# Kernel optimization log

Measured on AMD Instinct MI355X. Metric: run time of the kernel, lower is better.

## Reference

```python
import jax, jax.numpy as jnp
import numpy as np

N_BATCH, N_SEQ, N_CHANNELS = 32, 4096, 128
N_EXPERTS, TOP_K = 64, 2
D_IN = 2 * N_SEQ  # linear input width


def setup_inputs() -> dict:
    key = jax.random.key(0)
    k_x, k_wm, k_bm, k_wn, k_bn = jax.random.split(key, 5)
    scale = 1.0 / np.sqrt(D_IN)  # torch nn.Linear default init range
    return {
        "x": jax.random.normal(k_x, (N_BATCH, N_SEQ, N_CHANNELS, 2), dtype=jnp.float32),
        "W_main": jax.random.uniform(k_wm, (N_EXPERTS, D_IN), jnp.float32, -scale, scale),
        "b_main": jax.random.uniform(k_bm, (N_EXPERTS,), jnp.float32, -scale, scale),
        "W_noise": jax.random.uniform(k_wn, (N_EXPERTS, D_IN), jnp.float32, -scale, scale),
        "b_noise": jax.random.uniform(k_bn, (N_EXPERTS,), jnp.float32, -scale, scale),
    }


def _keep_top_k(logits, k):
    # torch.kthvalue(x, n-k) = (n-k)-th smallest (1-based) = sorted[:, n-k-1]
    n = logits.shape[1]
    if n < k:
        return logits
    kth = jnp.sort(logits, axis=1)[:, n - k - 1:n - k]  # [rows, 1]
    return jnp.where(logits > kth, logits, -jnp.inf)


def reference(x, W_main, b_main, W_noise, b_noise):
    n_batch, n_seq, n_channels, _ = x.shape
    # swapaxes(1,2) then reshape -> rows=[batch*channels], feat=[seq*2]
    x_r = jnp.swapaxes(x, 1, 2).reshape(n_batch * n_channels, 2 * n_seq)
    main_out = x_r @ W_main.T + b_main                      # [rows, E]
    noise_out = jax.nn.softplus(x_r @ W_noise.T + b_noise)  # [rows, E]
    gate = _keep_top_k(main_out + noise_out, TOP_K)
    return jax.nn.softmax(gate, axis=1)
```

## Files before the change

### kernel.cpp

```cpp
#include <hip/hip_runtime.h>
#include <cmath>

typedef _Float16 f16x8 __attribute__((ext_vector_type(8)));
typedef _Float16 f16x4 __attribute__((ext_vector_type(4)));
typedef float    f32x16 __attribute__((ext_vector_type(16)));

constexpr int NBATCH = 32;
constexpr int NSEQ   = 4096;
constexpr int NCH    = 128;
constexpr int NEXP   = 64;
constexpr int NE2    = 128;
constexpr int DIN    = 2 * NSEQ;
constexpr int ROWS   = NBATCH * NCH;
constexpr int KCH    = 16;
constexpr int KT     = 16;
constexpr float LOSC = 2048.0f;
constexpr float INV_LOSC = 1.0f / 2048.0f;

constexpr size_t WS_WHI = 32ull << 20;
constexpr size_t WS_WLO = 34ull << 20;

__device__ __forceinline__ int swz_f16(int row, int g) {
    return row * 32 + ((g ^ ((row >> 1) & 3)) << 3);
}

__device__ __forceinline__ void gload_lds16(const void* g, void* l) {
    __builtin_amdgcn_global_load_lds(
        (const __attribute__((address_space(1))) unsigned int*)g,
        (__attribute__((address_space(3))) unsigned int*)l, 16, 0, 0);
}

__global__ __launch_bounds__(256)
void wprep_kernel(const float* __restrict__ Wm, const float* __restrict__ Wn,
                  _Float16* __restrict__ Whi, _Float16* __restrict__ Wlo)
{
    const int idx = (blockIdx.x * 256 + threadIdx.x) * 4;
    const int row = idx >> 13;
    const int f   = idx & 8191;
    const float* src = (row < NEXP) ? (Wm + (size_t)row * DIN + f)
                                    : (Wn + (size_t)(row - NEXP) * DIN + f);
    const float4 v = *(const float4*)src;
    const int g  = (f >> 3) & 3;
    const int fs = (f & ~0x18) | ((g ^ ((row >> 1) & 3)) << 3);
    float vv[4] = { v.x, v.y, v.z, v.w };
    f16x4 h, l;
#pragma unroll
    for (int j = 0; j < 4; ++j) {
        _Float16 hj = (_Float16)vv[j];
        h[j] = hj;
        l[j] = (_Float16)((vv[j] - (float)hj) * LOSC);
    }
    *(f16x4*)&Whi[(size_t)row * 8192 + fs] = h;
    *(f16x4*)&Wlo[(size_t)row * 8192 + fs] = l;
}

__global__ __launch_bounds__(256, 2)
void gemm_kernel(const float* __restrict__ x,
                 const _Float16* __restrict__ Whi,
                 const _Float16* __restrict__ Wlo,
                 float* __restrict__ partials)
{
    const int l    = blockIdx.x;
    const int slot = l >> 3;
    const int kc   = (l & 7) + 8 * (slot & 1);
    const int b    = slot >> 1;

    const int tid  = threadIdx.x;
    const int lane = tid & 63;
    const int wave = tid >> 6;
    const int wm   = wave >> 1;
    const int wn   = wave & 1;

    __shared__ _Float16 lds[2 * 16384];

    f32x16 acc1[2][2], acc2[2][2];
#pragma unroll
    for (int mi = 0; mi < 2; ++mi)
#pragma unroll
        for (int ni = 0; ni < 2; ++ni)
#pragma unroll
            for (int r = 0; r < 16; ++r) { acc1[mi][ni][r] = 0.f; acc2[mi][ni][r] = 0.f; }

    const float* xchunk = x + (size_t)b * (NSEQ * 256) + (size_t)kc * (256 * 256);
    const int c    = tid & 127;
    const int gsel = tid >> 7;
    const int fb0  = kc * 512;

    const int e_ld = lane >> 2;
    const int goff = (lane & 3) * 8;

    float2 xr[8];
    auto load_x = [&](int t) {
#pragma unroll
        for (int u = 0; u < 2; ++u) {
            const int g = u * 2 + gsel;
#pragma unroll
            for (int i = 0; i < 4; ++i)
                xr[u * 4 + i] = *(const float2*)(xchunk + (size_t)(t * 16 + g * 4 + i) * 256 + c * 2);
        }
    };
    auto write_x = [&](int buf) {
        _Float16* Ah = lds + buf * 16384;
        _Float16* Al = Ah + 4096;
#pragma unroll
        for (int u = 0; u < 2; ++u) {
            const int g = u * 2 + gsel;
            f16x8 h, lo;
#pragma unroll
            for (int i = 0; i < 4; ++i) {
                float a0 = xr[u * 4 + i].x, a1 = xr[u * 4 + i].y;
                _Float16 h0 = (_Float16)a0, h1 = (_Float16)a1;
                h[2 * i] = h0; h[2 * i + 1] = h1;
                lo[2 * i]     = (_Float16)((a0 - (float)h0) * LOSC);
                lo[2 * i + 1] = (_Float16)((a1 - (float)h1) * LOSC);
            }
            const int off = swz_f16(c, g);
            *(f16x8*)&Ah[off] = h;
            *(f16x8*)&Al[off] = lo;
        }
    };
    auto issue_W = [&](int t, int buf) {
        const int fb = fb0 + t * 32;
        _Float16* Bh = lds + buf * 16384 + 8192;
        _Float16* Bl = Bh + 4096;
#pragma unroll
        for (int q = 0; q < 2; ++q) {
            const int e0 = wave * 32 + q * 16;
            gload_lds16(Whi + (size_t)(e0 + e_ld) * 8192 + fb + goff, Bh + e0 * 32);
            gload_lds16(Wlo + (size_t)(e0 + e_ld) * 8192 + fb + goff, Bl + e0 * 32);
        }
    };

    issue_W(0, 0);
    load_x(0);
    write_x(0);
    __syncthreads();

    for (int t = 0; t < KT; ++t) {
        const int buf = t & 1;
        if (t < KT - 1) { issue_W(t + 1, buf ^ 1); load_x(t + 1); }

        const _Float16* Ah = lds + buf * 16384;
        const _Float16* Al = Ah + 4096;
        const _Float16* Bh = Ah + 8192;
        const _Float16* Bl = Ah + 12288;
#pragma unroll
        for (int kk = 0; kk < 2; ++kk) {
            const int gk = kk * 2 + (lane >> 5);
            f16x8 ah[2], al[2], bh[2], bl[2];
#pragma unroll
            for (int i = 0; i < 2; ++i) {
                const int oa = swz_f16(wm * 64 + i * 32 + (lane & 31), gk);
                const int ob = swz_f16(wn * 64 + i * 32 + (lane & 31), gk);
                ah[i] = *(const f16x8*)&Ah[oa];
                al[i] = *(const f16x8*)&Al[oa];
                bh[i] = *(const f16x8*)&Bh[ob];
                bl[i] = *(const f16x8*)&Bl[ob];
            }
#pragma unroll
            for (int mi = 0; mi < 2; ++mi)
#pragma unroll
                for (int ni = 0; ni < 2; ++ni) {
                    acc1[mi][ni] = __builtin_amdgcn_mfma_f32_32x32x16_f16(ah[mi], bh[ni], acc1[mi][ni], 0, 0, 0);
                    acc2[mi][ni] = __builtin_amdgcn_mfma_f32_32x32x16_f16(ah[mi], bl[ni], acc2[mi][ni], 0, 0, 0);
                    acc2[mi][ni] = __builtin_amdgcn_mfma_f32_32x32x16_f16(al[mi], bh[ni], acc2[mi][ni], 0, 0, 0);
                }
        }
        if (t < KT - 1) write_x(buf ^ 1);
        __syncthreads();
    }

    float* outp = partials + ((size_t)kc * ROWS + (size_t)b * NCH) * NE2;
#pragma unroll
    for (int mi = 0; mi < 2; ++mi)
#pragma unroll
        for (int ni = 0; ni < 2; ++ni)
#pragma unroll
            for (int r = 0; r < 16; ++r) {
                const int rloc = (r & 3) + 8 * (r >> 2) + 4 * (lane >> 5);
                const int crow = wm * 64 + mi * 32 + rloc;
                const int e    = wn * 64 + ni * 32 + (lane & 31);
                outp[(size_t)crow * NE2 + e] = acc1[mi][ni][r] + acc2[mi][ni][r] * INV_LOSC;
            }
}

__global__ __launch_bounds__(256)
void gate_kernel(const float* __restrict__ partials,
                 const float* __restrict__ bm,
                 const float* __restrict__ bn,
                 float* __restrict__ out)
{
    const int tid  = threadIdx.x;
    const int rl   = tid >> 7;
    const int e    = tid & 127;
    const int lane = tid & 63;
    const int row  = blockIdx.x * 2 + rl;

    const float* p = partials + (size_t)row * NE2 + e;
    float s = 0.f;
#pragma unroll
    for (int kc = 0; kc < KCH; ++kc)
        s += p[(size_t)kc * ROWS * NE2];

    __shared__ float spl[2][64];
    if (e >= NEXP) {
        float nz = s + bn[lane];
        spl[rl][lane] = fmaxf(nz, 0.f) + log1pf(expf(-fabsf(nz)));
    }
    __syncthreads();
    if (e < NEXP) {
        float g = s + bm[lane] + spl[rl][lane];

        float v  = g;
        float m1 = v;
#pragma unroll
        for (int o = 32; o > 0; o >>= 1) m1 = fmaxf(m1, __shfl_xor(m1, o));
        unsigned long long b1 = __ballot(v == m1);
        int l1 = __ffsll(b1) - 1;
        if (lane == l1) v = -INFINITY;
        float m2 = v;
#pragma unroll
        for (int o = 32; o > 0; o >>= 1) m2 = fmaxf(m2, __shfl_xor(m2, o));
        unsigned long long b2 = __ballot(v == m2);
        int l2 = __ffsll(b2) - 1;
        if (lane == l2) v = -INFINITY;
        float kth = v;
#pragma unroll
        for (int o = 32; o > 0; o >>= 1) kth = fmaxf(kth, __shfl_xor(kth, o));

        float ev  = (g > kth) ? expf(g - m1) : 0.f;
        float den = ev;
#pragma unroll
        for (int o = 32; o > 0; o >>= 1) den += __shfl_xor(den, o);
        out[(size_t)row * NEXP + lane] = ev / den;
    }
}

extern "C" void kernel_launch(void* const* d_in, const int* in_sizes, int n_in,
                              void* d_out, int out_size, void* d_ws, size_t ws_size,
                              hipStream_t stream)
{
    const float* x  = (const float*)d_in[0];
    const float* Wm = (const float*)d_in[1];
    const float* bm = (const float*)d_in[2];
    const float* Wn = (const float*)d_in[3];
    const float* bn = (const float*)d_in[4];
    float* out      = (float*)d_out;

    float*     partials = (float*)d_ws;
    _Float16*  Whi      = (_Float16*)((char*)d_ws + WS_WHI);
    _Float16*  Wlo      = (_Float16*)((char*)d_ws + WS_WLO);

    wprep_kernel<<<1024, 256, 0, stream>>>(Wm, Wn, Whi, Wlo);
    gemm_kernel<<<512, 256, 0, stream>>>(x, Whi, Wlo, partials);
    gate_kernel<<<ROWS / 2, 256, 0, stream>>>(partials, bm, bn, out);
}
```

Before: 210.3 us.

## Deepen x register prefetch to two tiles with manual waitcnt barriers

Double-buffers the x register staging so global loads for tile t+2 are issued while tile t computes. The __syncthreads calls are replaced with explicit s_waitcnt vmcnt/lgkmcnt plus s_barrier and sched_barrier, so the newest loads stay outstanding across the barrier. The main loop is also fully unrolled. This is meant to hide global load latency for x, at the cost of more registers and reliance on hand-counted vmcnt values being correct.

```diff
diff --git a/kernel.cpp b/kernel.cpp
--- a/kernel.cpp
+++ b/kernel.cpp
@@ -85,21 +85,21 @@
     const int c    = tid & 127;
     const int gsel = tid >> 7;
     const int fb0  = kc * 512;
-
     const int e_ld = lane >> 2;
     const int goff = (lane & 3) * 8;
 
-    float2 xr[8];
-    auto load_x = [&](int t) {
+    float2 xr[2][8];
+
+    auto load_x = [&](int t, float2 (&dst)[8]) {
 #pragma unroll
         for (int u = 0; u < 2; ++u) {
             const int g = u * 2 + gsel;
 #pragma unroll
             for (int i = 0; i < 4; ++i)
-                xr[u * 4 + i] = *(const float2*)(xchunk + (size_t)(t * 16 + g * 4 + i) * 256 + c * 2);
+                dst[u * 4 + i] = *(const float2*)(xchunk + (size_t)(t * 16 + g * 4 + i) * 256 + c * 2);
         }
     };
-    auto write_x = [&](int buf) {
+    auto write_x = [&](int buf, float2 (&src)[8]) {
         _Float16* Ah = lds + buf * 16384;
         _Float16* Al = Ah + 4096;
 #pragma unroll
@@ -108,7 +108,7 @@
             f16x8 h, lo;
 #pragma unroll
             for (int i = 0; i < 4; ++i) {
-                float a0 = xr[u * 4 + i].x, a1 = xr[u * 4 + i].y;
+                float a0 = src[u * 4 + i].x, a1 = src[u * 4 + i].y;
                 _Float16 h0 = (_Float16)a0, h1 = (_Float16)a1;
                 h[2 * i] = h0; h[2 * i + 1] = h1;
                 lo[2 * i]     = (_Float16)((a0 - (float)h0) * LOSC);
@@ -132,13 +132,20 @@
     };
 
     issue_W(0, 0);
-    load_x(0);
-    write_x(0);
-    __syncthreads();
-
+    load_x(0, xr[0]);
+    load_x(1, xr[1]);
+    write_x(0, xr[0]);
+    asm volatile("s_waitcnt lgkmcnt(0)" ::: "memory");
+    __builtin_amdgcn_s_barrier();
+    __builtin_amdgcn_sched_barrier(0);
+
+#pragma unroll
     for (int t = 0; t < KT; ++t) {
         const int buf = t & 1;
-        if (t < KT - 1) { issue_W(t + 1, buf ^ 1); load_x(t + 1); }
+
+        if (t + 1 < KT) issue_W(t + 1, buf ^ 1);
+        if (t + 2 < KT) load_x(t + 2, xr[buf]);
+        __builtin_amdgcn_sched_barrier(0);
 
         const _Float16* Ah = lds + buf * 16384;
         const _Float16* Al = Ah + 4096;
@@ -166,8 +173,14 @@
                     acc2[mi][ni] = __builtin_amdgcn_mfma_f32_32x32x16_f16(al[mi], bh[ni], acc2[mi][ni], 0, 0, 0);
                 }
         }
-        if (t < KT - 1) write_x(buf ^ 1);
-        __syncthreads();
+
+        if (t + 1 < KT) {
+            write_x(buf ^ 1, xr[buf ^ 1]);
+            if (t + 2 < KT) asm volatile("s_waitcnt vmcnt(8) lgkmcnt(0)" ::: "memory");
+            else            asm volatile("s_waitcnt vmcnt(0) lgkmcnt(0)" ::: "memory");
+            __builtin_amdgcn_s_barrier();
+            __builtin_amdgcn_sched_barrier(0);
+        }
     }
 
     float* outp = partials + ((size_t)kc * ROWS + (size_t)b * NCH) * NE2;
```

New measurement: 211.4 us. No clear change (+0.5%).
